# Kernel optimization log

Hardware: AMD Instinct MI355X
Metric: run time of the kernel (lower is better)

Reference implementation:

```python
import jax, jax.numpy as jnp
import numpy as np

N_ENT = 50000
N_REL = 500
N_DIM = 256
K = 4            # num_blocks; n_arity = 3 -> arch has K**3 = 64 entries
B = 1024


def setup_inputs() -> dict:
    key = jax.random.key(0)
    k0, k1, k2, k3 = jax.random.split(key, 4)
    facts = jax.random.randint(k0, (B, 3), 0, N_REL)          # head, tail, rela (all < n_rel <= n_ent)
    arch = jax.random.randint(k1, (K ** 3,), 0, 3)            # selects op in {0, 1, -1}
    ent_w = jax.random.normal(k2, (N_ENT, N_DIM), dtype=jnp.float32) * 0.05  # xavier-ish scale
    rel_w = jax.random.normal(k3, (N_REL, N_DIM), dtype=jnp.float32) * 0.05
    return {
        "facts": facts,
        "arch": arch,
        "ent_w": ent_w,
        "rel_w": rel_w,
        "bne_gamma": jnp.ones((N_DIM,), jnp.float32),
        "bne_beta": jnp.zeros((N_DIM,), jnp.float32),
        "bnr_gamma": jnp.ones((N_DIM,), jnp.float32),
        "bnr_beta": jnp.zeros((N_DIM,), jnp.float32),
    }


def _bn(x, gamma, beta, eps=1e-5):
    # BatchNorm1d in training mode: biased batch statistics over the batch dim.
    m = jnp.mean(x, axis=0)
    v = jnp.var(x, axis=0)
    return (x - m) * jax.lax.rsqrt(v + eps) * gamma + beta


def _bce(p, y):
    # torch F.binary_cross_entropy clamps log terms at -100
    logp = jnp.maximum(jnp.log(p), -100.0)
    log1mp = jnp.maximum(jnp.log1p(-p), -100.0)
    return -jnp.mean(y * logp + (1.0 - y) * log1mp)


def reference(facts, arch, ent_w, rel_w, bne_gamma, bne_beta, bnr_gamma, bnr_beta):
    L = N_DIM // K
    h, t, r = facts[:, 0], facts[:, 1], facts[:, 2]
    # separate BN calls for head / tail batches, as in the torch code (dropout is eval-mode identity)
    he = _bn(ent_w[h], bne_gamma, bne_beta).reshape(-1, K, L)   # [B, K, L]
    te = _bn(ent_w[t], bne_gamma, bne_beta).reshape(-1, K, L)
    re = _bn(rel_w[r], bnr_gamma, bnr_beta).reshape(-1, K, L)
    # alpha[i,j,k] = ops[op_idx[i*K*K + j*K + k]] in {0, 1, -1}
    alpha = jnp.asarray([0.0, 1.0, -1.0], dtype=ent_w.dtype)[arch].reshape(K, K, K)
    # fused extend + inner_vec + inner_alpha_bi + sum-over-blocks:
    # last_idx=2 (head side, rela x tail): vec[b,k,l] = sum_{i,j} alpha[i,j,k] r[b,i,l] t[b,j,l]
    head_vec = jnp.einsum('ijk,bil,bjl->bkl', alpha, re, te).reshape(-1, N_DIM)
    # last_idx=1 (tail side, rela x head): vec[b,k,l] = sum_{i,j} alpha[i,k,j] r[b,i,l] h[b,j,l]
    tail_vec = jnp.einsum('ikj,bil,bjl->bkl', alpha, re, he).reshape(-1, N_DIM)
    head_p = jax.nn.softmax(head_vec @ ent_w.T, axis=1)         # [B, N_ENT]
    tail_p = jax.nn.softmax(tail_vec @ ent_w.T, axis=1)
    head_label = jax.nn.one_hot(h, N_ENT, dtype=head_p.dtype)
    tail_label = jax.nn.one_hot(t, N_ENT, dtype=tail_p.dtype)
    return _bce(head_p, head_label) + _bce(tail_p, tail_label)
```

## Files before the change

### kernel.cpp

```cpp
#include <hip/hip_runtime.h>

#define N_ENT   50000
#define N_ENT_P 50176
#define NDIM    256
#define BATCH   1024
#define MROWS   2048
#define BMT     256
#define BKT     64
#define NTILES  196
#define NSTRIP  32
#define SHIFT   30.0f

typedef __attribute__((ext_vector_type(8))) short short8;
typedef __attribute__((ext_vector_type(4))) float f32x4;

__device__ __forceinline__ unsigned short f2bf(float f) {
  unsigned int u = __float_as_uint(f);
  u += 0x7fffu + ((u >> 16) & 1u);
  return (unsigned short)(u >> 16);
}

__device__ __forceinline__ void async16(const void* g, void* lds) {
  __builtin_amdgcn_global_load_lds(
      (const __attribute__((address_space(1))) unsigned int*)g,
      (__attribute__((address_space(3))) unsigned int*)lds,
      16, 0, 0);
}

__global__ void k_prep(const float* __restrict__ ent_w,
                       unsigned short* __restrict__ Wb,
                       const int* __restrict__ facts,
                       const float* __restrict__ rel_w,
                       float* __restrict__ stats) {
  if (blockIdx.x < (N_ENT_P * 64) / 256) {
    int t = blockIdx.x * 256 + threadIdx.x;
    int row = t >> 6, c4 = (t & 63) << 2;
    ushort4 v;
    if (row < N_ENT) {
      float4 f = *(const float4*)(ent_w + row * NDIM + c4);
      v.x = f2bf(f.x); v.y = f2bf(f.y); v.z = f2bf(f.z); v.w = f2bf(f.w);
    } else {
      v.x = v.y = v.z = v.w = 0;
    }
    *(ushort4*)(Wb + row * NDIM + c4) = v;
  } else {
    int sb = blockIdx.x - (N_ENT_P * 64) / 256;
    int seg = sb >> 6;
    int d = threadIdx.x;
    const float* tab = (seg == 2) ? rel_w : ent_w;
    int r0 = (sb & 63) * 16;
    int idxs[16];
#pragma unroll
    for (int i = 0; i < 16; ++i) idxs[i] = facts[(r0 + i) * 3 + seg];
    float s = 0.f, s2 = 0.f;
#pragma unroll
    for (int i = 0; i < 16; ++i) {
      float v = tab[idxs[i] * NDIM + d];
      s += v; s2 += v * v;
    }
    atomicAdd(&stats[(seg * 2 + 0) * NDIM + d], s);
    atomicAdd(&stats[(seg * 2 + 1) * NDIM + d], s2);
  }
}

__global__ void k_vectors(const int* __restrict__ facts, const int* __restrict__ arch,
                          const float* __restrict__ ent_w, const float* __restrict__ rel_w,
                          const float* __restrict__ bne_g, const float* __restrict__ bne_b,
                          const float* __restrict__ bnr_g, const float* __restrict__ bnr_b,
                          const float* __restrict__ stats,
                          unsigned short* __restrict__ HVb, float* __restrict__ zlab) {
  __shared__ float sh_he[256], sh_te[256], sh_re[256], sh_alpha[64], sh_red[16];
  int b = blockIdx.x, d = threadIdx.x;
  int h = facts[b * 3 + 0], t = facts[b * 3 + 1], r = facts[b * 3 + 2];
  const float inv = 1.0f / (float)BATCH;
  float mh = stats[0 * 256 + d] * inv, vh = stats[1 * 256 + d] * inv - mh * mh;
  float mt = stats[2 * 256 + d] * inv, vt = stats[3 * 256 + d] * inv - mt * mt;
  float mr = stats[4 * 256 + d] * inv, vr = stats[5 * 256 + d] * inv - mr * mr;
  float sch = rsqrtf(vh + 1e-5f) * bne_g[d], shh = bne_b[d] - mh * sch;
  float sct = rsqrtf(vt + 1e-5f) * bne_g[d], sht = bne_b[d] - mt * sct;
  float scr = rsqrtf(vr + 1e-5f) * bnr_g[d], shr = bnr_b[d] - mr * scr;
  sh_he[d] = ent_w[h * NDIM + d] * sch + shh;
  sh_te[d] = ent_w[t * NDIM + d] * sct + sht;
  sh_re[d] = rel_w[r * NDIM + d] * scr + shr;
  if (d < 64) {
    int a = arch[d];
    sh_alpha[d] = (a == 0) ? 0.f : ((a == 1) ? 1.f : -1.f);
  }
  __syncthreads();
  int k = d >> 6, l = d & 63;
  float hv = 0.f, tv = 0.f;
#pragma unroll
  for (int i = 0; i < 4; ++i) {
    float re_i = sh_re[i * 64 + l];
#pragma unroll
    for (int j = 0; j < 4; ++j) {
      hv += sh_alpha[i * 16 + j * 4 + k] * re_i * sh_te[j * 64 + l];
      tv += sh_alpha[i * 16 + k * 4 + j] * re_i * sh_he[j * 64 + l];
    }
  }
  HVb[b * NDIM + d] = f2bf(hv);
  HVb[(BATCH + b) * NDIM + d] = f2bf(tv);
  float ph = hv * ent_w[h * NDIM + d];
  float pt = tv * ent_w[t * NDIM + d];
  for (int m = 1; m < 64; m <<= 1) { ph += __shfl_xor(ph, m); pt += __shfl_xor(pt, m); }
  int wid = d >> 6;
  if ((d & 63) == 0) { sh_red[wid] = ph; sh_red[8 + wid] = pt; }
  __syncthreads();
  if (d == 0) {
    zlab[b] = sh_red[0] + sh_red[1] + sh_red[2] + sh_red[3];
    zlab[BATCH + b] = sh_red[8] + sh_red[9] + sh_red[10] + sh_red[11];
  }
}

__global__ void __launch_bounds__(512, 2)
k_gemm(const unsigned short* __restrict__ HVb, const unsigned short* __restrict__ Wb,
       float* __restrict__ m1, float* __restrict__ m2) {
  __shared__ __align__(16) unsigned short As[2][BMT * BKT];
  __shared__ __align__(16) unsigned short Bs[2][BMT * BKT];
  __shared__ float part[2][8][128];
  const int tid = threadIdx.x;
  const int lane = tid & 63, wid = tid >> 6;
  const int L = blockIdx.x;
  const int s = (L >> 6) * 8 + (L & 7);
  const int bm = ((L >> 3) & 7) * BMT;
  const int wm = (wid >> 2) * 128, wn = (wid & 3) * 64;
  const int q = lane >> 4, ln = lane & 15;
  const int ntmine = NTILES / NSTRIP + (s < (NTILES % NSTRIP) ? 1 : 0);
  const int njobs = ntmine * 4;

  const int srow0 = tid >> 3;
  const int skg = (((tid & 7) ^ (srow0 & 7)) << 3);
  const int abase = (wm + ln) * 128;
  const int bbase = (wn + ln) * 128;
  const int k0x = ((q ^ (ln & 7)) << 4);
  const int k1x = (((4 + q) ^ (ln & 7)) << 4);

  auto stage = [&](int j) {
    int jj = (j < njobs) ? j : j - 2;
    int nt = jj >> 2, kt = jj & 3, buf = jj & 1;
    const unsigned short* Ag = HVb + (size_t)(bm + srow0) * NDIM + kt * 64 + skg;
    const unsigned short* Bg = Wb +
        (size_t)((s + nt * NSTRIP) * 256 + srow0) * NDIM + kt * 64 + skg;
    char* Ad = (char*)As[buf] + tid * 16;
    char* Bd = (char*)Bs[buf] + tid * 16;
#pragma unroll
    for (int i = 0; i < 4; ++i) {
      async16(Ag + i * (64 * NDIM), Ad + i * 8192);
      async16(Bg + i * (64 * NDIM), Bd + i * 8192);
    }
  };

  float ps1[8][4] = {}, ps2[8][4] = {};

  stage(0); stage(1);
  asm volatile("s_waitcnt vmcnt(8)" ::: "memory");
  __builtin_amdgcn_s_barrier();

  for (int nt = 0; nt < ntmine; ++nt) {
    f32x4 acc[8][4] = {};
#pragma unroll
    for (int kt = 0; kt < 4; ++kt) {
      const char* Ab = (const char*)As[kt & 1];
      const char* Bb = (const char*)Bs[kt & 1];
#pragma unroll
      for (int kh = 0; kh < 2; ++kh) {
        const int kx = kh ? k1x : k0x;
        short8 fb[4];
#pragma unroll
        for (int ni = 0; ni < 4; ++ni)
          fb[ni] = *(const short8*)(Bb + bbase + ni * 2048 + kx);
#pragma unroll
        for (int mi = 0; mi < 8; ++mi) {
          short8 fa = *(const short8*)(Ab + abase + mi * 2048 + kx);
          __builtin_amdgcn_s_setprio(1);
#pragma unroll
          for (int ni = 0; ni < 4; ++ni)
            acc[mi][ni] = __builtin_amdgcn_mfma_f32_16x16x32_bf16(
                fa, fb[ni], acc[mi][ni], 0, 0, 0);
          __builtin_amdgcn_s_setprio(0);
        }
      }
      asm volatile("s_waitcnt lgkmcnt(0)" ::: "memory");
      __builtin_amdgcn_s_barrier();
      stage(nt * 4 + kt + 2);
      asm volatile("s_waitcnt vmcnt(8)" ::: "memory");
      __builtin_amdgcn_s_barrier();
    }
#pragma unroll
    for (int mi = 0; mi < 8; ++mi)
#pragma unroll
      for (int reg = 0; reg < 4; ++reg) {
        float a1 = 0.f, a2 = 0.f;
#pragma unroll
        for (int ni = 0; ni < 4; ++ni) {
          float e = __expf(acc[mi][ni][reg] - SHIFT);
          a1 += e; a2 += e * e;
        }
        ps1[mi][reg] += a1; ps2[mi][reg] += a2;
      }
  }
  asm volatile("s_waitcnt vmcnt(0)" ::: "memory");

#pragma unroll
  for (int mi = 0; mi < 8; ++mi)
#pragma unroll
    for (int reg = 0; reg < 4; ++reg) {
      float a1 = ps1[mi][reg], a2 = ps2[mi][reg];
      for (int m = 1; m < 16; m <<= 1) { a1 += __shfl_xor(a1, m); a2 += __shfl_xor(a2, m); }
      if (ln == 0) {
        part[0][wid][mi * 16 + q * 4 + reg] = a1;
        part[1][wid][mi * 16 + q * 4 + reg] = a2;
      }
    }
  __syncthreads();
  {
    int kind = tid >> 8, rl = tid & 255;
    int w0 = (rl >> 7) * 4, rr = rl & 127;
    float v = part[kind][w0][rr] + part[kind][w0 + 1][rr] +
              part[kind][w0 + 2][rr] + part[kind][w0 + 3][rr];
    atomicAdd((kind ? m2 : m1) + bm + rl, v);
  }
}

__global__ void k_finalize(const float* __restrict__ m1, const float* __restrict__ m2,
                           const float* __restrict__ zlab, float* __restrict__ out) {
  __shared__ float red[16];
  int tid = threadIdx.x;
  float local = 0.f;
  for (int r = tid; r < MROWS; r += 1024) {
    float M1 = m1[r];
    float lse = SHIFT + logf(M1);
    float zl = zlab[r];
    float lp = fmaxf(zl - lse, -100.f);
    float pl = __expf(zl - lse);
    float l1m = fmaxf(log1pf(-pl), -100.f);
    float iM1 = 1.f / M1;
    float r2 = m2[r] * iM1 * iM1;
    float series = -(1.f + 0.5f * r2);
    local += lp - l1m + series;
  }
  for (int m = 1; m < 64; m <<= 1) local += __shfl_xor(local, m);
  if ((tid & 63) == 0) red[tid >> 6] = local;
  __syncthreads();
  if (tid == 0) {
    float s = 0.f;
    for (int i = 0; i < 16; ++i) s += red[i];
    out[0] = -s / ((float)BATCH * (float)N_ENT);
  }
}

extern "C" void kernel_launch(void* const* d_in, const int* in_sizes, int n_in,
                              void* d_out, int out_size, void* d_ws, size_t ws_size,
                              hipStream_t stream) {
  const int* facts = (const int*)d_in[0];
  const int* arch = (const int*)d_in[1];
  const float* ent_w = (const float*)d_in[2];
  const float* rel_w = (const float*)d_in[3];
  const float* bne_g = (const float*)d_in[4];
  const float* bne_b = (const float*)d_in[5];
  const float* bnr_g = (const float*)d_in[6];
  const float* bnr_b = (const float*)d_in[7];
  char* ws = (char*)d_ws;
  float* stats = (float*)ws;
  float* m1 = (float*)(ws + 6144);
  float* m2 = (float*)(ws + 14336);
  float* zlab = (float*)(ws + 22528);
  unsigned short* HVb = (unsigned short*)(ws + 30720);
  unsigned short* Wb = (unsigned short*)(ws + 30720 + 1048576);

  hipMemsetAsync(ws, 0, 22528, stream);
  k_prep<<<dim3((N_ENT_P * 64) / 256 + 192), dim3(256), 0, stream>>>(
      ent_w, Wb, facts, rel_w, stats);
  k_vectors<<<dim3(BATCH), dim3(256), 0, stream>>>(facts, arch, ent_w, rel_w,
                                                   bne_g, bne_b, bnr_g, bnr_b,
                                                   stats, HVb, zlab);
  k_gemm<<<dim3(256), dim3(512), 0, stream>>>(HVb, Wb, m1, m2);
  k_finalize<<<dim3(1), dim3(1024), 0, stream>>>(m1, m2, zlab, (float*)d_out);
}
```

Measured before the change: 214.6 us.

## Software-pipeline LDS fragment loads in GEMM and fuse finalize via last-block reduction

The GEMM inner loop now prefetches A/B register fragments for the next half-step while the MFMAs for the current half run, with sched barriers to keep that ordering. Per-tile softmax partial sums are reduced across lanes straight into shared memory, which removes the 64 persistent accumulator registers; launch bounds are relaxed to one block per SIMD set. The separate finalize kernel is removed: the last block, detected with an atomic counter, computes the loss. This drops one launch but adds a threadfence and atomics, and may lower occupancy.

```diff
diff --git a/kernel.cpp b/kernel.cpp
--- a/kernel.cpp
+++ b/kernel.cpp
@@ -112,12 +112,16 @@
   }
 }
 
-__global__ void __launch_bounds__(512, 2)
+__global__ void __launch_bounds__(512, 1)
 k_gemm(const unsigned short* __restrict__ HVb, const unsigned short* __restrict__ Wb,
-       float* __restrict__ m1, float* __restrict__ m2) {
+       float* __restrict__ m1, float* __restrict__ m2,
+       const float* __restrict__ zlab, unsigned int* __restrict__ cnt,
+       float* __restrict__ out) {
   __shared__ __align__(16) unsigned short As[2][BMT * BKT];
   __shared__ __align__(16) unsigned short Bs[2][BMT * BKT];
   __shared__ float part[2][8][128];
+  __shared__ float sred[8];
+  __shared__ int slast;
   const int tid = threadIdx.x;
   const int lane = tid & 63, wid = tid >> 6;
   const int L = blockIdx.x;
@@ -128,12 +132,18 @@
   const int ntmine = NTILES / NSTRIP + (s < (NTILES % NSTRIP) ? 1 : 0);
   const int njobs = ntmine * 4;
 
+  ((float*)part)[tid] = 0.f; ((float*)part)[512 + tid] = 0.f;
+  ((float*)part)[1024 + tid] = 0.f; ((float*)part)[1536 + tid] = 0.f;
+
   const int srow0 = tid >> 3;
   const int skg = (((tid & 7) ^ (srow0 & 7)) << 3);
-  const int abase = (wm + ln) * 128;
-  const int bbase = (wn + ln) * 128;
-  const int k0x = ((q ^ (ln & 7)) << 4);
-  const int k1x = (((4 + q) ^ (ln & 7)) << 4);
+  int aoffL[4], aoffH[4], boff0[4];
+#pragma unroll
+  for (int f = 0; f < 4; ++f) {
+    aoffL[f] = (wm + f * 16 + ln) * 128 + ((q ^ (ln & 7)) << 4);
+    aoffH[f] = (wm + (4 + f) * 16 + ln) * 128 + ((q ^ (ln & 7)) << 4);
+    boff0[f] = (wn + f * 16 + ln) * 128 + ((q ^ (ln & 7)) << 4);
+  }
 
   auto stage = [&](int j) {
     int jj = (j < njobs) ? j : j - 2;
@@ -150,41 +160,58 @@
     }
   };
 
-  float ps1[8][4] = {}, ps2[8][4] = {};
+#define MMA4(FA, FB, MO)                                                      \
+  __builtin_amdgcn_s_setprio(1);                                              \
+  _Pragma("unroll") for (int mi = 0; mi < 4; ++mi)                            \
+      _Pragma("unroll") for (int ni = 0; ni < 4; ++ni)                        \
+          acc[(MO) + mi][ni] = __builtin_amdgcn_mfma_f32_16x16x32_bf16(       \
+              FA[mi], FB[ni], acc[(MO) + mi][ni], 0, 0, 0);                   \
+  __builtin_amdgcn_s_setprio(0);
+
+  short8 faA[4], faB[4], fbA[4], fbB[4];
 
   stage(0); stage(1);
   asm volatile("s_waitcnt vmcnt(8)" ::: "memory");
   __builtin_amdgcn_s_barrier();
+#pragma unroll
+  for (int f = 0; f < 4; ++f) faA[f] = *(const short8*)((const char*)As[0] + aoffL[f]);
+#pragma unroll
+  for (int f = 0; f < 4; ++f) fbA[f] = *(const short8*)((const char*)Bs[0] + boff0[f]);
 
   for (int nt = 0; nt < ntmine; ++nt) {
     f32x4 acc[8][4] = {};
 #pragma unroll
     for (int kt = 0; kt < 4; ++kt) {
-      const char* Ab = (const char*)As[kt & 1];
-      const char* Bb = (const char*)Bs[kt & 1];
-#pragma unroll
-      for (int kh = 0; kh < 2; ++kh) {
-        const int kx = kh ? k1x : k0x;
-        short8 fb[4];
-#pragma unroll
-        for (int ni = 0; ni < 4; ++ni)
-          fb[ni] = *(const short8*)(Bb + bbase + ni * 2048 + kx);
-#pragma unroll
-        for (int mi = 0; mi < 8; ++mi) {
-          short8 fa = *(const short8*)(Ab + abase + mi * 2048 + kx);
-          __builtin_amdgcn_s_setprio(1);
-#pragma unroll
-          for (int ni = 0; ni < 4; ++ni)
-            acc[mi][ni] = __builtin_amdgcn_mfma_f32_16x16x32_bf16(
-                fa, fb[ni], acc[mi][ni], 0, 0, 0);
-          __builtin_amdgcn_s_setprio(0);
-        }
-      }
+      const int p = kt & 1;
+      const char* Ap = (const char*)As[p];
+      const char* Bp = (const char*)Bs[p];
+      const char* An = (const char*)As[p ^ 1];
+      const char* Bn = (const char*)Bs[p ^ 1];
+#pragma unroll
+      for (int f = 0; f < 4; ++f) faB[f] = *(const short8*)(Ap + aoffH[f]);
+#pragma unroll
+      for (int f = 0; f < 4; ++f) fbB[f] = *(const short8*)(Bp + (boff0[f] ^ 64));
+      __builtin_amdgcn_sched_barrier(0);
+      MMA4(faA, fbA, 0)
+#pragma unroll
+      for (int f = 0; f < 4; ++f) faA[f] = *(const short8*)(Ap + (aoffL[f] ^ 64));
+      __builtin_amdgcn_sched_barrier(0);
+      MMA4(faB, fbA, 4)
+#pragma unroll
+      for (int f = 0; f < 4; ++f) faB[f] = *(const short8*)(Ap + (aoffH[f] ^ 64));
+      __builtin_amdgcn_sched_barrier(0);
+      MMA4(faA, fbB, 0)
       asm volatile("s_waitcnt lgkmcnt(0)" ::: "memory");
       __builtin_amdgcn_s_barrier();
       stage(nt * 4 + kt + 2);
       asm volatile("s_waitcnt vmcnt(8)" ::: "memory");
       __builtin_amdgcn_s_barrier();
+#pragma unroll
+      for (int f = 0; f < 4; ++f) faA[f] = *(const short8*)(An + aoffL[f]);
+#pragma unroll
+      for (int f = 0; f < 4; ++f) fbA[f] = *(const short8*)(Bn + boff0[f]);
+      __builtin_amdgcn_sched_barrier(0);
+      MMA4(faB, fbB, 4)
     }
 #pragma unroll
     for (int mi = 0; mi < 8; ++mi)
@@ -196,22 +223,15 @@
           float e = __expf(acc[mi][ni][reg] - SHIFT);
           a1 += e; a2 += e * e;
         }
-        ps1[mi][reg] += a1; ps2[mi][reg] += a2;
+        for (int m = 1; m < 16; m <<= 1) { a1 += __shfl_xor(a1, m); a2 += __shfl_xor(a2, m); }
+        if (ln == 0) {
+          part[0][wid][mi * 16 + q * 4 + reg] += a1;
+          part[1][wid][mi * 16 + q * 4 + reg] += a2;
+        }
       }
   }
+#undef MMA4
   asm volatile("s_waitcnt vmcnt(0)" ::: "memory");
-
-#pragma unroll
-  for (int mi = 0; mi < 8; ++mi)
-#pragma unroll
-    for (int reg = 0; reg < 4; ++reg) {
-      float a1 = ps1[mi][reg], a2 = ps2[mi][reg];
-      for (int m = 1; m < 16; m <<= 1) { a1 += __shfl_xor(a1, m); a2 += __shfl_xor(a2, m); }
-      if (ln == 0) {
-        part[0][wid][mi * 16 + q * 4 + reg] = a1;
-        part[1][wid][mi * 16 + q * 4 + reg] = a2;
-      }
-    }
   __syncthreads();
   {
     int kind = tid >> 8, rl = tid & 255;
@@ -220,32 +240,33 @@
               part[kind][w0 + 2][rr] + part[kind][w0 + 3][rr];
     atomicAdd((kind ? m2 : m1) + bm + rl, v);
   }
-}
-
-__global__ void k_finalize(const float* __restrict__ m1, const float* __restrict__ m2,
-                           const float* __restrict__ zlab, float* __restrict__ out) {
-  __shared__ float red[16];
-  int tid = threadIdx.x;
-  float local = 0.f;
-  for (int r = tid; r < MROWS; r += 1024) {
-    float M1 = m1[r];
-    float lse = SHIFT + logf(M1);
-    float zl = zlab[r];
-    float lp = fmaxf(zl - lse, -100.f);
-    float pl = __expf(zl - lse);
-    float l1m = fmaxf(log1pf(-pl), -100.f);
-    float iM1 = 1.f / M1;
-    float r2 = m2[r] * iM1 * iM1;
-    float series = -(1.f + 0.5f * r2);
-    local += lp - l1m + series;
-  }
-  for (int m = 1; m < 64; m <<= 1) local += __shfl_xor(local, m);
-  if ((tid & 63) == 0) red[tid >> 6] = local;
+  __threadfence();
+  if (tid == 0) slast = (atomicAdd(cnt, 1u) + 1u == 256u) ? 1 : 0;
   __syncthreads();
-  if (tid == 0) {
-    float s = 0.f;
-    for (int i = 0; i < 16; ++i) s += red[i];
-    out[0] = -s / ((float)BATCH * (float)N_ENT);
+  if (slast) {
+    __threadfence();
+    float local = 0.f;
+    for (int r = tid; r < MROWS; r += 512) {
+      float M1 = __hip_atomic_load(&m1[r], __ATOMIC_RELAXED, __HIP_MEMORY_SCOPE_AGENT);
+      float M2 = __hip_atomic_load(&m2[r], __ATOMIC_RELAXED, __HIP_MEMORY_SCOPE_AGENT);
+      float lse = SHIFT + logf(M1);
+      float zl = zlab[r];
+      float lp = fmaxf(zl - lse, -100.f);
+      float pl = __expf(zl - lse);
+      float l1m = fmaxf(log1pf(-pl), -100.f);
+      float iM1 = 1.f / M1;
+      float r2 = M2 * iM1 * iM1;
+      float series = -(1.f + 0.5f * r2);
+      local += lp - l1m + series;
+    }
+    for (int m = 1; m < 64; m <<= 1) local += __shfl_xor(local, m);
+    if ((tid & 63) == 0) sred[tid >> 6] = local;
+    __syncthreads();
+    if (tid == 0) {
+      float ssum = 0.f;
+      for (int i = 0; i < 8; ++i) ssum += sred[i];
+      out[0] = -ssum / ((float)BATCH * (float)N_ENT);
+    }
   }
 }
 
@@ -264,16 +285,17 @@
   float* stats = (float*)ws;
   float* m1 = (float*)(ws + 6144);
   float* m2 = (float*)(ws + 14336);
-  float* zlab = (float*)(ws + 22528);
-  unsigned short* HVb = (unsigned short*)(ws + 30720);
-  unsigned short* Wb = (unsigned short*)(ws + 30720 + 1048576);
-
-  hipMemsetAsync(ws, 0, 22528, stream);
+  unsigned int* cnt = (unsigned int*)(ws + 22528);
+  float* zlab = (float*)(ws + 24576);
+  unsigned short* HVb = (unsigned short*)(ws + 32768);
+  unsigned short* Wb = (unsigned short*)(ws + 32768 + 1048576);
+
+  hipMemsetAsync(ws, 0, 22544, stream);
   k_prep<<<dim3((N_ENT_P * 64) / 256 + 192), dim3(256), 0, stream>>>(
       ent_w, Wb, facts, rel_w, stats);
   k_vectors<<<dim3(BATCH), dim3(256), 0, stream>>>(facts, arch, ent_w, rel_w,
                                                    bne_g, bne_b, bnr_g, bnr_b,
                                                    stats, HVb, zlab);
-  k_gemm<<<dim3(256), dim3(512), 0, stream>>>(HVb, Wb, m1, m2);
-  k_finalize<<<dim3(1), dim3(1024), 0, stream>>>(m1, m2, zlab, (float*)d_out);
-}
+  k_gemm<<<dim3(256), dim3(512), 0, stream>>>(HVb, Wb, m1, m2, zlab, cnt,
+                                              (float*)d_out);
+}
```

Result: slower. 255.5 us (+19.1%).
